# Kernel optimization log

Measured on AMD Instinct MI355X. Metric: run time of the kernel, lower is better.

Reference implementation:

```python
import jax, jax.numpy as jnp
import numpy as np

TOTAL_DIM = 64  # 16+16+16+8+8
HIDDEN = 4 * TOTAL_DIM
NUM_HEADS = 8


def _fourier(x, num_freqs):
    # Dyadic Fourier features: sin/cos of 2^j * x for j in [0, num_freqs).
    # Output dim = input_dim * num_freqs * 2 (matches embed_dim in the module).
    freqs = 2.0 ** jnp.arange(num_freqs, dtype=x.dtype)  # (F,)
    phase = x[..., :, None] * freqs                       # (..., in, F)
    out = jnp.concatenate([jnp.sin(phase), jnp.cos(phase)], axis=-1)  # (..., in, 2F)
    return out.reshape(x.shape[:-1] + (-1,))


def setup_inputs() -> dict:
    key = jax.random.key(0)
    k1, k2, k3, k4, k5, k6 = jax.random.split(key, 6)
    B, Nq, Nk, D = 8, 256, 256, 10
    query_states = jax.random.normal(k1, (B, Nq, D), dtype=jnp.float32)
    key_states = jax.random.normal(k2, (B, Nk, D), dtype=jnp.float32)
    W1 = jax.random.normal(k3, (TOTAL_DIM, HIDDEN), dtype=jnp.float32) / np.sqrt(TOTAL_DIM)
    b1 = jnp.zeros((HIDDEN,), dtype=jnp.float32)
    W2 = jax.random.normal(k4, (HIDDEN, NUM_HEADS), dtype=jnp.float32) / np.sqrt(HIDDEN)
    b2 = jnp.zeros((NUM_HEADS,), dtype=jnp.float32)
    return {"query_states": query_states, "key_states": key_states,
            "W1": W1, "b1": b1, "W2": W2, "b2": b2}


def _features(query_states, key_states):
    # Slice per-ship fields, then broadcast pairwise: q -> (B,Nq,1,*), k -> (B,1,Nk,*)
    q_team = query_states[:, :, None, 0]          # (B,Nq,1)
    k_team = key_states[:, None, :, 0]            # (B,1,Nk)
    q_pos = query_states[:, :, None, 3:5]
    k_pos = key_states[:, None, :, 3:5]
    q_vel = query_states[:, :, None, 5:7]
    k_vel = key_states[:, None, :, 5:7]
    q_att = query_states[:, :, None, 7:9]
    k_att = key_states[:, None, :, 7:9]

    delta_pos = k_pos - q_pos                     # (B,Nq,Nk,2)
    delta_vel = k_vel - q_vel                     # (B,Nq,Nk,2)
    feat_delta_input = jnp.concatenate([delta_pos, delta_vel], axis=-1)  # (B,Nq,Nk,4)

    dist_sq = jnp.sum(delta_pos ** 2, axis=-1, keepdims=True)
    dist = jnp.sqrt(dist_sq + 1e-6)
    inv_dist = 1.0 / (dist + 0.1)
    feat_dist_input = jnp.concatenate([dist, inv_dist], axis=-1)         # (B,Nq,Nk,2)

    bearing = delta_pos / (dist + 1e-6)
    ata = jnp.sum(bearing * q_att, axis=-1, keepdims=True)
    aspect = jnp.sum(bearing * k_att, axis=-1, keepdims=True)
    feat_angle_input = jnp.concatenate([ata, aspect], axis=-1)           # (B,Nq,Nk,2)

    dot_dp_dv = jnp.sum(delta_pos * delta_vel, axis=-1, keepdims=True)
    speed_sq = jnp.sum(delta_vel ** 2, axis=-1, keepdims=True)
    ttca = jnp.tanh(jax.nn.relu(-dot_dp_dv / (speed_sq + 1e-6)))
    feat_intercept_input = jnp.concatenate([ttca, dist], axis=-1)        # (B,Nq,Nk,2)

    same_team = (q_team == k_team).astype(query_states.dtype)[..., None]
    q_speed = jnp.linalg.norm(q_vel, axis=-1, keepdims=True)
    k_speed = jnp.linalg.norm(k_vel, axis=-1, keepdims=True)
    delta_speed = k_speed - q_speed
    feat_team_input = jnp.concatenate([same_team, delta_speed], axis=-1)  # (B,Nq,Nk,2)

    out_dist = _fourier(feat_dist_input, 4)        # 16
    out_angle = _fourier(feat_angle_input, 4)      # 16
    out_delta = _fourier(feat_delta_input, 2)      # 16
    out_intercept = _fourier(feat_intercept_input, 2)  # 8
    out_team = _fourier(feat_team_input, 2)        # 8
    return jnp.concatenate([out_dist, out_angle, out_delta, out_intercept, out_team], axis=-1)


def reference(query_states, key_states, W1, b1, W2, b2):
    combined = _features(query_states, key_states)          # (B,Nq,Nk,64)
    h = jax.nn.silu(combined @ W1 + b1)                     # (B,Nq,Nk,256)
    bias = h @ W2 + b2                                      # (B,Nq,Nk,H)
    return jnp.transpose(bias, (0, 3, 1, 2))                # (B,H,Nq,Nk)
```

## Files before the change

kernel.cpp:

```cpp
#include <hip/hip_runtime.h>
#include <math.h>

#define NB 8
#define NQ 256
#define NK 256
#define DIN 10
#define FDIM 64
#define HIDDEN 256
#define NH 8

#define FSTRIDE 64
#define HSTRIDE 264
#define W2S 264

typedef float f32x4 __attribute__((ext_vector_type(4)));
typedef short bf16x8 __attribute__((ext_vector_type(8)));

__device__ __forceinline__ short f2bf(float f) {
    return (short)((__float_as_uint(f) + 0x8000u) >> 16);
}
__device__ __forceinline__ unsigned pack2(float a, float b) {
    unsigned ua = __float_as_uint(a) + 0x8000u;
    unsigned ub = __float_as_uint(b) + 0x8000u;
    return __builtin_amdgcn_perm(ub, ua, 0x07060302);
}

__device__ __forceinline__ void four4(float x, float* dst) {
    float s1 = __sinf(x), c1 = __cosf(x);
    float s2 = 2.f * s1 * c1, c2 = 1.f - 2.f * s1 * s1;
    float s4 = 2.f * s2 * c2, c4 = 1.f - 2.f * s2 * s2;
    float s8 = 2.f * s4 * c4, c8 = 1.f - 2.f * s4 * s4;
    dst[0] = s1; dst[1] = s2; dst[2] = s4; dst[3] = s8;
    dst[4] = c1; dst[5] = c2; dst[6] = c4; dst[7] = c8;
}
__device__ __forceinline__ void four2(float x, float* dst) {
    float s1 = __sinf(x), c1 = __cosf(x);
    dst[0] = s1; dst[1] = 2.f * s1 * c1;
    dst[2] = c1; dst[3] = 1.f - 2.f * s1 * s1;
}

__global__ __launch_bounds__(256, 2) void relfeat_mfma_kernel(
    const float* __restrict__ q, const float* __restrict__ k,
    const float* __restrict__ W1, const float* __restrict__ b1,
    const float* __restrict__ W2, const float* __restrict__ b2,
    float* __restrict__ out)
{
    __shared__ __align__(16) short feat_s[NK * FSTRIDE];
    __shared__ __align__(16) short h_s[64 * HSTRIDE];
    __shared__ __align__(16) short w2_s[8 * W2S];

    const int t = threadIdx.x;
    const int wave = t >> 6;
    const int lane15 = t & 15;
    const int quad = (t >> 4) & 3;
    const int b = blockIdx.x >> 8;
    const int i = blockIdx.x & (NQ - 1);

    {
        const float* kp = k + ((size_t)b * NK + t) * DIN;
        const float k0 = kp[0], k3 = kp[3], k4 = kp[4], k5 = kp[5], k6 = kp[6],
                    k7 = kp[7], k8 = kp[8];
        const float* qp = q + ((size_t)b * NQ + i) * DIN;
        const float q0 = qp[0], q3 = qp[3], q4 = qp[4], q5 = qp[5], q6 = qp[6],
                    q7 = qp[7], q8 = qp[8];

        const float dpx = k3 - q3, dpy = k4 - q4;
        const float dvx = k5 - q5, dvy = k6 - q6;
        const float dist = sqrtf(dpx * dpx + dpy * dpy + 1e-6f);
        const float inv_dist = 1.0f / (dist + 0.1f);
        const float inv_d2 = 1.0f / (dist + 1e-6f);
        const float bear_x = dpx * inv_d2, bear_y = dpy * inv_d2;
        const float ata = bear_x * q7 + bear_y * q8;
        const float aspect = bear_x * k7 + bear_y * k8;
        const float dot_dp_dv = dpx * dvx + dpy * dvy;
        const float speed_sq = dvx * dvx + dvy * dvy;
        const float ttca = tanhf(fmaxf(0.f, -dot_dp_dv / (speed_sq + 1e-6f)));
        const float same_team = (q0 == k0) ? 1.f : 0.f;
        const float q_speed = sqrtf(q5 * q5 + q6 * q6);
        const float k_speed = sqrtf(k5 * k5 + k6 * k6);
        const float delta_speed = k_speed - q_speed;

        float feat[FDIM];
        four4(dist,        feat + 0);
        four4(inv_dist,    feat + 8);
        four4(ata,         feat + 16);
        four4(aspect,      feat + 24);
        four2(dpx,         feat + 32);
        four2(dpy,         feat + 36);
        four2(dvx,         feat + 40);
        four2(dvy,         feat + 44);
        four2(ttca,        feat + 48);
        four2(dist,        feat + 52);
        four2(same_team,   feat + 56);
        four2(delta_speed, feat + 60);

        const int sw = t & 7;
#pragma unroll
        for (int c8 = 0; c8 < 8; ++c8) {
            uint4 v;
            v.x = pack2(feat[c8 * 8 + 0], feat[c8 * 8 + 1]);
            v.y = pack2(feat[c8 * 8 + 2], feat[c8 * 8 + 3]);
            v.z = pack2(feat[c8 * 8 + 4], feat[c8 * 8 + 5]);
            v.w = pack2(feat[c8 * 8 + 6], feat[c8 * 8 + 7]);
            *(uint4*)&feat_s[t * FSTRIDE + ((c8 ^ sw) * 8)] = v;
        }
    }

#pragma unroll
    for (int o = 0; o < NH; ++o) w2_s[o * W2S + t] = f2bf(W2[t * NH + o]);

    const int n0 = wave * 64;
    bf16x8 w1f[4][2];
#pragma unroll
    for (int nt = 0; nt < 4; ++nt)
#pragma unroll
        for (int ks = 0; ks < 2; ++ks) {
            const float* wp = W1 + (size_t)(ks * 32 + quad * 8) * HIDDEN
                              + (n0 + nt * 16 + lane15);
            bf16x8 v;
#pragma unroll
            for (int e = 0; e < 8; ++e) v[e] = f2bf(wp[(size_t)e * HIDDEN]);
            w1f[nt][ks] = v;
        }
    float4 b1q[4];
#pragma unroll
    for (int nt = 0; nt < 4; ++nt)
        b1q[nt] = *(const float4*)&b1[n0 + nt * 16 + quad * 4];
    const float b2v = (lane15 < NH) ? b2[lane15] : 0.f;

    __syncthreads();

    const int swr = lane15 & 7;
#pragma unroll 1
    for (int c = 0; c < 4; ++c) {
        const int p0 = c * 64;

        f32x4 acc[4][4];
#pragma unroll
        for (int nt = 0; nt < 4; ++nt)
#pragma unroll
            for (int mt = 0; mt < 4; ++mt)
                acc[nt][mt] = (f32x4){b1q[nt].x, b1q[nt].y, b1q[nt].z, b1q[nt].w};
#pragma unroll
        for (int ks = 0; ks < 2; ++ks)
#pragma unroll
            for (int mt = 0; mt < 4; ++mt) {
                const int row = p0 + mt * 16 + lane15;
                const bf16x8 fb = *(const bf16x8*)
                    &feat_s[row * FSTRIDE + (((ks * 4 + quad) ^ swr) * 8)];
#pragma unroll
                for (int nt = 0; nt < 4; ++nt)
                    acc[nt][mt] = __builtin_amdgcn_mfma_f32_16x16x32_bf16(
                        w1f[nt][ks], fb, acc[nt][mt], 0, 0, 0);
            }

        __syncthreads();

#pragma unroll
        for (int nt = 0; nt < 4; ++nt)
#pragma unroll
            for (int mt = 0; mt < 4; ++mt) {
                const int pair = mt * 16 + lane15;
                const int hbase = n0 + nt * 16 + quad * 4;
                float s[4];
#pragma unroll
                for (int r = 0; r < 4; ++r) {
                    const float pv = acc[nt][mt][r];
                    const float e = __builtin_amdgcn_exp2f(pv * -1.44269504f);
                    s[r] = pv * __builtin_amdgcn_rcpf(1.f + e);
                }
                uint2 pk;
                pk.x = pack2(s[0], s[1]);
                pk.y = pack2(s[2], s[3]);
                *(uint2*)&h_s[pair * HSTRIDE + hbase] = pk;
            }
        __syncthreads();

        {
            const int pw = wave * 16;
            f32x4 acc2 = (f32x4){b2v, b2v, b2v, b2v};
#pragma unroll
            for (int ks = 0; ks < 8; ++ks) {
                const bf16x8 ha = *(const bf16x8*)&h_s[(pw + lane15) * HSTRIDE
                                                        + ks * 32 + quad * 8];
                const bf16x8 wb = *(const bf16x8*)&w2_s[(lane15 & 7) * W2S
                                                         + ks * 32 + quad * 8];
                acc2 = __builtin_amdgcn_mfma_f32_16x16x32_bf16(ha, wb, acc2, 0, 0, 0);
            }
            if (lane15 < NH) {
                float* op = out + (((size_t)b * NH + lane15) * NQ + i) * NK
                            + (p0 + pw + quad * 4);
                *(float4*)op = make_float4(acc2[0], acc2[1], acc2[2], acc2[3]);
            }
        }
    }
}

extern "C" void kernel_launch(void* const* d_in, const int* in_sizes, int n_in,
                              void* d_out, int out_size, void* d_ws, size_t ws_size,
                              hipStream_t stream) {
    const float* q  = (const float*)d_in[0];
    const float* k  = (const float*)d_in[1];
    const float* W1 = (const float*)d_in[2];
    const float* b1 = (const float*)d_in[3];
    const float* W2 = (const float*)d_in[4];
    const float* b2 = (const float*)d_in[5];
    float* out = (float*)d_out;

    dim3 grid(NB * NQ);
    dim3 block(NK);
    relfeat_mfma_kernel<<<grid, block, 0, stream>>>(q, k, W1, b1, W2, b2, out);
}
```

Baseline: 116.3 us.

## Process four query rows per block and fold log2e scaling into weights

Each block now handles four query rows instead of one, so the W1 and W2 bf16 conversion, the bias loads and the key-state loads are amortised over four rows, and the grid shrinks by four. W1, b1 and W2 are prescaled by -log2(e) and -ln(2), so the SiLU uses exp2 directly on the accumulator without an extra multiply. Prescaling before bf16 rounding changes numerics slightly. Per-block work becomes serial over rows with an extra barrier per row, which cuts block-level parallelism to 512 blocks.

```diff
diff --git a/kernel.cpp b/kernel.cpp
--- a/kernel.cpp
+++ b/kernel.cpp
@@ -8,6 +8,7 @@
 #define FDIM 64
 #define HIDDEN 256
 #define NH 8
+#define ROWS_PER_BLK 4
 
 #define FSTRIDE 64
 #define HSTRIDE 264
@@ -53,61 +54,16 @@
     const int wave = t >> 6;
     const int lane15 = t & 15;
     const int quad = (t >> 4) & 3;
-    const int b = blockIdx.x >> 8;
-    const int i = blockIdx.x & (NQ - 1);
-
-    {
-        const float* kp = k + ((size_t)b * NK + t) * DIN;
-        const float k0 = kp[0], k3 = kp[3], k4 = kp[4], k5 = kp[5], k6 = kp[6],
-                    k7 = kp[7], k8 = kp[8];
-        const float* qp = q + ((size_t)b * NQ + i) * DIN;
-        const float q0 = qp[0], q3 = qp[3], q4 = qp[4], q5 = qp[5], q6 = qp[6],
-                    q7 = qp[7], q8 = qp[8];
-
-        const float dpx = k3 - q3, dpy = k4 - q4;
-        const float dvx = k5 - q5, dvy = k6 - q6;
-        const float dist = sqrtf(dpx * dpx + dpy * dpy + 1e-6f);
-        const float inv_dist = 1.0f / (dist + 0.1f);
-        const float inv_d2 = 1.0f / (dist + 1e-6f);
-        const float bear_x = dpx * inv_d2, bear_y = dpy * inv_d2;
-        const float ata = bear_x * q7 + bear_y * q8;
-        const float aspect = bear_x * k7 + bear_y * k8;
-        const float dot_dp_dv = dpx * dvx + dpy * dvy;
-        const float speed_sq = dvx * dvx + dvy * dvy;
-        const float ttca = tanhf(fmaxf(0.f, -dot_dp_dv / (speed_sq + 1e-6f)));
-        const float same_team = (q0 == k0) ? 1.f : 0.f;
-        const float q_speed = sqrtf(q5 * q5 + q6 * q6);
-        const float k_speed = sqrtf(k5 * k5 + k6 * k6);
-        const float delta_speed = k_speed - q_speed;
-
-        float feat[FDIM];
-        four4(dist,        feat + 0);
-        four4(inv_dist,    feat + 8);
-        four4(ata,         feat + 16);
-        four4(aspect,      feat + 24);
-        four2(dpx,         feat + 32);
-        four2(dpy,         feat + 36);
-        four2(dvx,         feat + 40);
-        four2(dvy,         feat + 44);
-        four2(ttca,        feat + 48);
-        four2(dist,        feat + 52);
-        four2(same_team,   feat + 56);
-        four2(delta_speed, feat + 60);
-
-        const int sw = t & 7;
-#pragma unroll
-        for (int c8 = 0; c8 < 8; ++c8) {
-            uint4 v;
-            v.x = pack2(feat[c8 * 8 + 0], feat[c8 * 8 + 1]);
-            v.y = pack2(feat[c8 * 8 + 2], feat[c8 * 8 + 3]);
-            v.z = pack2(feat[c8 * 8 + 4], feat[c8 * 8 + 5]);
-            v.w = pack2(feat[c8 * 8 + 6], feat[c8 * 8 + 7]);
-            *(uint4*)&feat_s[t * FSTRIDE + ((c8 ^ sw) * 8)] = v;
-        }
-    }
-
-#pragma unroll
-    for (int o = 0; o < NH; ++o) w2_s[o * W2S + t] = f2bf(W2[t * NH + o]);
+    const int b = blockIdx.x >> 6;
+    const int i0 = (blockIdx.x & 63) * ROWS_PER_BLK;
+
+    const float* kp = k + ((size_t)b * NK + t) * DIN;
+    const float k0 = kp[0], k3 = kp[3], k4 = kp[4], k5 = kp[5], k6 = kp[6],
+                k7 = kp[7], k8 = kp[8];
+
+#pragma unroll
+    for (int o = 0; o < NH; ++o)
+        w2_s[o * W2S + t] = f2bf(-0.69314718f * W2[t * NH + o]);
 
     const int n0 = wave * 64;
     bf16x8 w1f[4][2];
@@ -119,78 +75,134 @@
                               + (n0 + nt * 16 + lane15);
             bf16x8 v;
 #pragma unroll
-            for (int e = 0; e < 8; ++e) v[e] = f2bf(wp[(size_t)e * HIDDEN]);
+            for (int e = 0; e < 8; ++e)
+                v[e] = f2bf(-1.44269504f * wp[(size_t)e * HIDDEN]);
             w1f[nt][ks] = v;
         }
     float4 b1q[4];
 #pragma unroll
-    for (int nt = 0; nt < 4; ++nt)
-        b1q[nt] = *(const float4*)&b1[n0 + nt * 16 + quad * 4];
+    for (int nt = 0; nt < 4; ++nt) {
+        float4 bb = *(const float4*)&b1[n0 + nt * 16 + quad * 4];
+        b1q[nt] = make_float4(-1.44269504f * bb.x, -1.44269504f * bb.y,
+                              -1.44269504f * bb.z, -1.44269504f * bb.w);
+    }
     const float b2v = (lane15 < NH) ? b2[lane15] : 0.f;
 
-    __syncthreads();
-
+    const int sw = t & 7;
     const int swr = lane15 & 7;
+
 #pragma unroll 1
-    for (int c = 0; c < 4; ++c) {
-        const int p0 = c * 64;
-
-        f32x4 acc[4][4];
-#pragma unroll
-        for (int nt = 0; nt < 4; ++nt)
-#pragma unroll
-            for (int mt = 0; mt < 4; ++mt)
-                acc[nt][mt] = (f32x4){b1q[nt].x, b1q[nt].y, b1q[nt].z, b1q[nt].w};
-#pragma unroll
-        for (int ks = 0; ks < 2; ++ks)
-#pragma unroll
-            for (int mt = 0; mt < 4; ++mt) {
-                const int row = p0 + mt * 16 + lane15;
-                const bf16x8 fb = *(const bf16x8*)
-                    &feat_s[row * FSTRIDE + (((ks * 4 + quad) ^ swr) * 8)];
-#pragma unroll
-                for (int nt = 0; nt < 4; ++nt)
-                    acc[nt][mt] = __builtin_amdgcn_mfma_f32_16x16x32_bf16(
-                        w1f[nt][ks], fb, acc[nt][mt], 0, 0, 0);
+    for (int row = 0; row < ROWS_PER_BLK; ++row) {
+        const int i = i0 + row;
+
+        {
+            const float* qp = q + ((size_t)b * NQ + i) * DIN;
+            const float q0 = qp[0], q3 = qp[3], q4 = qp[4], q5 = qp[5],
+                        q6 = qp[6], q7 = qp[7], q8 = qp[8];
+
+            const float dpx = k3 - q3, dpy = k4 - q4;
+            const float dvx = k5 - q5, dvy = k6 - q6;
+            const float dist = sqrtf(dpx * dpx + dpy * dpy + 1e-6f);
+            const float inv_dist = 1.0f / (dist + 0.1f);
+            const float inv_d2 = 1.0f / (dist + 1e-6f);
+            const float bear_x = dpx * inv_d2, bear_y = dpy * inv_d2;
+            const float ata = bear_x * q7 + bear_y * q8;
+            const float aspect = bear_x * k7 + bear_y * k8;
+            const float dot_dp_dv = dpx * dvx + dpy * dvy;
+            const float speed_sq = dvx * dvx + dvy * dvy;
+            const float ttca = tanhf(fmaxf(0.f, -dot_dp_dv / (speed_sq + 1e-6f)));
+            const float same_team = (q0 == k0) ? 1.f : 0.f;
+            const float q_speed = sqrtf(q5 * q5 + q6 * q6);
+            const float k_speed = sqrtf(k5 * k5 + k6 * k6);
+            const float delta_speed = k_speed - q_speed;
+
+            float feat[FDIM];
+            four4(dist,        feat + 0);
+            four4(inv_dist,    feat + 8);
+            four4(ata,         feat + 16);
+            four4(aspect,      feat + 24);
+            four2(dpx,         feat + 32);
+            four2(dpy,         feat + 36);
+            four2(dvx,         feat + 40);
+            four2(dvy,         feat + 44);
+            four2(ttca,        feat + 48);
+            four2(dist,        feat + 52);
+            four2(same_team,   feat + 56);
+            four2(delta_speed, feat + 60);
+
+#pragma unroll
+            for (int c8 = 0; c8 < 8; ++c8) {
+                uint4 v;
+                v.x = pack2(feat[c8 * 8 + 0], feat[c8 * 8 + 1]);
+                v.y = pack2(feat[c8 * 8 + 2], feat[c8 * 8 + 3]);
+                v.z = pack2(feat[c8 * 8 + 4], feat[c8 * 8 + 5]);
+                v.w = pack2(feat[c8 * 8 + 6], feat[c8 * 8 + 7]);
+                *(uint4*)&feat_s[t * FSTRIDE + ((c8 ^ sw) * 8)] = v;
             }
-
+        }
         __syncthreads();
 
-#pragma unroll
-        for (int nt = 0; nt < 4; ++nt)
-#pragma unroll
-            for (int mt = 0; mt < 4; ++mt) {
-                const int pair = mt * 16 + lane15;
-                const int hbase = n0 + nt * 16 + quad * 4;
-                float s[4];
-#pragma unroll
-                for (int r = 0; r < 4; ++r) {
-                    const float pv = acc[nt][mt][r];
-                    const float e = __builtin_amdgcn_exp2f(pv * -1.44269504f);
-                    s[r] = pv * __builtin_amdgcn_rcpf(1.f + e);
-                }
-                uint2 pk;
-                pk.x = pack2(s[0], s[1]);
-                pk.y = pack2(s[2], s[3]);
-                *(uint2*)&h_s[pair * HSTRIDE + hbase] = pk;
-            }
-        __syncthreads();
-
-        {
-            const int pw = wave * 16;
-            f32x4 acc2 = (f32x4){b2v, b2v, b2v, b2v};
-#pragma unroll
-            for (int ks = 0; ks < 8; ++ks) {
-                const bf16x8 ha = *(const bf16x8*)&h_s[(pw + lane15) * HSTRIDE
-                                                        + ks * 32 + quad * 8];
-                const bf16x8 wb = *(const bf16x8*)&w2_s[(lane15 & 7) * W2S
-                                                         + ks * 32 + quad * 8];
-                acc2 = __builtin_amdgcn_mfma_f32_16x16x32_bf16(ha, wb, acc2, 0, 0, 0);
-            }
-            if (lane15 < NH) {
-                float* op = out + (((size_t)b * NH + lane15) * NQ + i) * NK
-                            + (p0 + pw + quad * 4);
-                *(float4*)op = make_float4(acc2[0], acc2[1], acc2[2], acc2[3]);
+#pragma unroll 1
+        for (int c = 0; c < 4; ++c) {
+            const int p0 = c * 64;
+
+            f32x4 acc[4][4];
+#pragma unroll
+            for (int nt = 0; nt < 4; ++nt)
+#pragma unroll
+                for (int mt = 0; mt < 4; ++mt)
+                    acc[nt][mt] = (f32x4){b1q[nt].x, b1q[nt].y, b1q[nt].z, b1q[nt].w};
+#pragma unroll
+            for (int ks = 0; ks < 2; ++ks)
+#pragma unroll
+                for (int mt = 0; mt < 4; ++mt) {
+                    const int r2 = p0 + mt * 16 + lane15;
+                    const bf16x8 fb = *(const bf16x8*)
+                        &feat_s[r2 * FSTRIDE + (((ks * 4 + quad) ^ swr) * 8)];
+#pragma unroll
+                    for (int nt = 0; nt < 4; ++nt)
+                        acc[nt][mt] = __builtin_amdgcn_mfma_f32_16x16x32_bf16(
+                            w1f[nt][ks], fb, acc[nt][mt], 0, 0, 0);
+                }
+
+            __syncthreads();
+
+#pragma unroll
+            for (int nt = 0; nt < 4; ++nt)
+#pragma unroll
+                for (int mt = 0; mt < 4; ++mt) {
+                    const int pair = mt * 16 + lane15;
+                    const int hbase = n0 + nt * 16 + quad * 4;
+                    float s[4];
+#pragma unroll
+                    for (int r = 0; r < 4; ++r) {
+                        const float a = acc[nt][mt][r];
+                        const float e = __builtin_amdgcn_exp2f(a);
+                        s[r] = a * __builtin_amdgcn_rcpf(1.f + e);
+                    }
+                    uint2 pk;
+                    pk.x = pack2(s[0], s[1]);
+                    pk.y = pack2(s[2], s[3]);
+                    *(uint2*)&h_s[pair * HSTRIDE + hbase] = pk;
+                }
+            __syncthreads();
+
+            {
+                const int pw = wave * 16;
+                f32x4 acc2 = (f32x4){b2v, b2v, b2v, b2v};
+#pragma unroll
+                for (int ks = 0; ks < 8; ++ks) {
+                    const bf16x8 ha = *(const bf16x8*)&h_s[(pw + lane15) * HSTRIDE
+                                                            + ks * 32 + quad * 8];
+                    const bf16x8 wb = *(const bf16x8*)&w2_s[(lane15 & 7) * W2S
+                                                             + ks * 32 + quad * 8];
+                    acc2 = __builtin_amdgcn_mfma_f32_16x16x32_bf16(ha, wb, acc2, 0, 0, 0);
+                }
+                if (lane15 < NH) {
+                    float* op = out + (((size_t)b * NH + lane15) * NQ + i) * NK
+                                + (p0 + pw + quad * 4);
+                    *(float4*)op = make_float4(acc2[0], acc2[1], acc2[2], acc2[3]);
+                }
             }
         }
     }
@@ -207,7 +219,7 @@
     const float* b2 = (const float*)d_in[5];
     float* out = (float*)d_out;
 
-    dim3 grid(NB * NQ);
+    dim3 grid(NB * NQ / ROWS_PER_BLK);
     dim3 block(NK);
     relfeat_mfma_kernel<<<grid, block, 0, stream>>>(q, k, W1, b1, W2, b2, out);
 }
```

New measurement: 113.3 us. 1.03x faster.
